# Kernel tuning notes

Measured on AMD Instinct MI355X. Metric: run time of the kernel, lower is better.

The kernel has to match this reference:

```python
import jax, jax.numpy as jnp
import numpy as np

NUM_FINE = 1048576
NUM_FEATURES = 128
TARGET_NUM_SEGMENTS = 262144


def setup_inputs() -> dict:
    key = jax.random.key(0)
    k1, k2 = jax.random.split(key)
    fine_scale_h_d = jax.random.normal(k1, (NUM_FINE, NUM_FEATURES), dtype=jnp.float32)
    prolongation_map_fine_to_coarse = jax.random.randint(
        k2, (NUM_FINE,), 0, TARGET_NUM_SEGMENTS, dtype=jnp.int32)
    return {
        "fine_scale_h_d": fine_scale_h_d,
        "prolongation_map_fine_to_coarse": prolongation_map_fine_to_coarse,
    }


def reference(fine_scale_h_d, prolongation_map_fine_to_coarse):
    # segment_mean = segment_sum / segment_count, with 0 for empty segments
    # (matches tf.math.segment_mean). No sort needed: segment_sum handles
    # unsorted ids via scatter-add, which is the math-equivalent single pass.
    seg_sum = jax.ops.segment_sum(
        fine_scale_h_d, prolongation_map_fine_to_coarse,
        num_segments=TARGET_NUM_SEGMENTS)  # [S, F]
    seg_cnt = jax.ops.segment_sum(
        jnp.ones((fine_scale_h_d.shape[0],), dtype=fine_scale_h_d.dtype),
        prolongation_map_fine_to_coarse,
        num_segments=TARGET_NUM_SEGMENTS)  # [S]
    denom = jnp.maximum(seg_cnt, 1.0)[:, None]
    return seg_sum / denom
```

## Files before the change

kernel.cpp:

```cpp
#include <hip/hip_runtime.h>

#define NUM_FINE 1048576
#define NF 128
#define NUM_SEG 262144

typedef float f32x4 __attribute__((ext_vector_type(4)));

__global__ void count_rank_kernel(const int* __restrict__ ids, int* __restrict__ cnt,
                                  int* __restrict__ rank) {
    int i = (blockIdx.x * blockDim.x + threadIdx.x) * 4;
    int4 a = *reinterpret_cast<const int4*>(ids + i);
    int4 r;
    r.x = atomicAdd(&cnt[a.x], 1);
    r.y = atomicAdd(&cnt[a.y], 1);
    r.z = atomicAdd(&cnt[a.z], 1);
    r.w = atomicAdd(&cnt[a.w], 1);
    *reinterpret_cast<int4*>(rank + i) = r;
}

__global__ void scan1_kernel(const int* __restrict__ cnt, int* __restrict__ base,
                             int* __restrict__ blockSums) {
    __shared__ int lds[256];
    int tid = threadIdx.x;
    int g = blockIdx.x * 1024 + tid * 4;
    int4 a = *reinterpret_cast<const int4*>(cnt + g);
    int s = a.x + a.y + a.z + a.w;
    lds[tid] = s;
    __syncthreads();
    for (int off = 1; off < 256; off <<= 1) {
        int v = (tid >= off) ? lds[tid - off] : 0;
        __syncthreads();
        lds[tid] += v;
        __syncthreads();
    }
    int excl = lds[tid] - s;
    int4 o;
    o.x = excl;
    o.y = o.x + a.x;
    o.z = o.y + a.y;
    o.w = o.z + a.z;
    *reinterpret_cast<int4*>(base + g) = o;
    if (tid == 255) blockSums[blockIdx.x] = lds[255];
}

__global__ void scan3_kernel(int* __restrict__ base, const int* __restrict__ blockSums,
                             const int* __restrict__ cnt, int2* __restrict__ desc) {
    __shared__ int lds[256];
    int tid = threadIdx.x;
    int v = blockSums[tid];
    lds[tid] = v;
    __syncthreads();
    for (int off = 1; off < 256; off <<= 1) {
        int t = (tid >= off) ? lds[tid - off] : 0;
        __syncthreads();
        lds[tid] += t;
        __syncthreads();
    }
    int add = (blockIdx.x > 0) ? lds[blockIdx.x - 1] : 0;
    int g = blockIdx.x * 1024 + tid * 4;
    int4 b = *reinterpret_cast<int4*>(base + g);
    int4 cc = *reinterpret_cast<const int4*>(cnt + g);
    b.x += add; b.y += add; b.z += add; b.w += add;
    *reinterpret_cast<int4*>(base + g) = b;
    *reinterpret_cast<int4*>(desc + g)     = make_int4(b.x, cc.x, b.y, cc.y);
    *reinterpret_cast<int4*>(desc + g + 2) = make_int4(b.z, cc.z, b.w, cc.w);
}

__global__ void place_kernel(const int* __restrict__ ids, const int* __restrict__ base,
                             const int* __restrict__ rank, int* __restrict__ perm) {
    int i = (blockIdx.x * blockDim.x + threadIdx.x) * 4;
    int4 a = *reinterpret_cast<const int4*>(ids + i);
    int4 r = *reinterpret_cast<const int4*>(rank + i);
    perm[base[a.x] + r.x] = i;
    perm[base[a.y] + r.y] = i + 1;
    perm[base[a.z] + r.z] = i + 2;
    perm[base[a.w] + r.w] = i + 3;
}

__device__ __forceinline__ f32x4 rowld(const float* __restrict__ x,
                                       const int* __restrict__ perm,
                                       int j, int end, int last, int f) {
    int jj = (j < end) ? j : last;
    int row = perm[jj];
    f32x4 v = *reinterpret_cast<const f32x4*>(x + (size_t)row * NF + f);
    float m = (j < end) ? 1.f : 0.f;
    return v * m;
}

__global__ void gather_kernel(const float* __restrict__ x,
                              const int* __restrict__ perm,
                              const int2* __restrict__ desc,
                              float* __restrict__ out) {
    int wid = (blockIdx.x << 2) | (threadIdx.x >> 6);
    int lane = threadIdx.x & 63;
    int h = lane >> 5;
    int f = (lane & 31) << 2;
    int2 d = desc[wid];
    int start = d.x, c = d.y;
    int end = start + c, last = end - 1;
    f32x4 acc = {0.f, 0.f, 0.f, 0.f};
    if (c > 0) {
        if (c <= 2) {
            acc = rowld(x, perm, start + h, end, last, f);
        } else if (c <= 4) {
            acc = rowld(x, perm, start + h,     end, last, f)
                + rowld(x, perm, start + 2 + h, end, last, f);
        } else if (c <= 8) {
            acc = rowld(x, perm, start + h,     end, last, f)
                + rowld(x, perm, start + 2 + h, end, last, f)
                + rowld(x, perm, start + 4 + h, end, last, f)
                + rowld(x, perm, start + 6 + h, end, last, f);
        } else {
            for (int r = start; r < end; r += 8) {
                acc += rowld(x, perm, r + h,     end, last, f)
                     + rowld(x, perm, r + 2 + h, end, last, f)
                     + rowld(x, perm, r + 4 + h, end, last, f)
                     + rowld(x, perm, r + 6 + h, end, last, f);
            }
        }
        acc.x += __shfl_xor(acc.x, 32);
        acc.y += __shfl_xor(acc.y, 32);
        acc.z += __shfl_xor(acc.z, 32);
        acc.w += __shfl_xor(acc.w, 32);
    }
    if (h == 0) {
        float inv = 1.0f / (float)(c > 1 ? c : 1);
        f32x4 o = acc * inv;
        *reinterpret_cast<f32x4*>(out + (size_t)wid * NF + f) = o;
    }
}

extern "C" void kernel_launch(void* const* d_in, const int* in_sizes, int n_in,
                              void* d_out, int out_size, void* d_ws, size_t ws_size,
                              hipStream_t stream) {
    const float* x   = (const float*)d_in[0];
    const int*   ids = (const int*)d_in[1];
    float* out = (float*)d_out;

    char* ws = (char*)d_ws;
    int*  cnt       = (int*)(ws);
    int*  base      = (int*)(ws + (1 << 20));
    int*  blockSums = (int*)(ws + (2 << 20));
    int*  perm      = (int*)(ws + (3 << 20));
    int*  rank      = (int*)(ws + (7 << 20));
    int2* desc      = (int2*)(ws + (11 << 20));

    hipMemsetAsync(cnt, 0, (size_t)NUM_SEG * sizeof(int), stream);

    count_rank_kernel<<<NUM_FINE / 1024, 256, 0, stream>>>(ids, cnt, rank);
    scan1_kernel<<<NUM_SEG / 1024, 256, 0, stream>>>(cnt, base, blockSums);
    scan3_kernel<<<NUM_SEG / 1024, 256, 0, stream>>>(base, blockSums, cnt, desc);
    place_kernel<<<NUM_FINE / 1024, 256, 0, stream>>>(ids, base, rank, perm);

    gather_kernel<<<NUM_SEG / 4, 256, 0, stream>>>(x, perm, desc, out);
}
```

Baseline: 209.8 us.

## Fuse counting, scan and placement into one cooperative kernel

Replaces the memset and the four setup kernels (count/rank, two scan passes, place) with a single cooperative kernel of 256 blocks × 512 threads that uses grid-wide syncs between phases. Ranks and ids stay in registers, so the rank array is no longer written to and read back from global memory. Launch overheads go away as well. A 5–6 row case is added to the gather branch to avoid one padded load. The trade-off is grid.sync costs and lower parallelism per phase, since each thread handles 8 ids.

```diff
diff --git a/kernel.cpp b/kernel.cpp
--- a/kernel.cpp
+++ b/kernel.cpp
@@ -1,80 +1,80 @@
 #include <hip/hip_runtime.h>
+#include <hip/hip_cooperative_groups.h>
+
+namespace cg = cooperative_groups;
 
 #define NUM_FINE 1048576
 #define NF 128
 #define NUM_SEG 262144
 
+#define SB 256
+#define ST 512
+
 typedef float f32x4 __attribute__((ext_vector_type(4)));
 
-__global__ void count_rank_kernel(const int* __restrict__ ids, int* __restrict__ cnt,
-                                  int* __restrict__ rank) {
-    int i = (blockIdx.x * blockDim.x + threadIdx.x) * 4;
-    int4 a = *reinterpret_cast<const int4*>(ids + i);
-    int4 r;
-    r.x = atomicAdd(&cnt[a.x], 1);
-    r.y = atomicAdd(&cnt[a.y], 1);
-    r.z = atomicAdd(&cnt[a.z], 1);
-    r.w = atomicAdd(&cnt[a.w], 1);
-    *reinterpret_cast<int4*>(rank + i) = r;
-}
+__global__ void fused_setup(const int* __restrict__ ids, int* __restrict__ cnt,
+                            int* __restrict__ blockSums, int* __restrict__ base,
+                            int* __restrict__ perm, int2* __restrict__ desc) {
+    cg::grid_group grid = cg::this_grid();
+    __shared__ int lds[ST];
+    const int tid = threadIdx.x, bid = blockIdx.x;
+    const int gt = bid * ST + tid;
 
-__global__ void scan1_kernel(const int* __restrict__ cnt, int* __restrict__ base,
-                             int* __restrict__ blockSums) {
-    __shared__ int lds[256];
-    int tid = threadIdx.x;
-    int g = blockIdx.x * 1024 + tid * 4;
-    int4 a = *reinterpret_cast<const int4*>(cnt + g);
-    int s = a.x + a.y + a.z + a.w;
+    *reinterpret_cast<int2*>(cnt + gt * 2) = make_int2(0, 0);
+
+    int myids[8];
+    const int ibase = gt * 8;
+    int4 a0 = *reinterpret_cast<const int4*>(ids + ibase);
+    int4 a1 = *reinterpret_cast<const int4*>(ids + ibase + 4);
+    myids[0] = a0.x; myids[1] = a0.y; myids[2] = a0.z; myids[3] = a0.w;
+    myids[4] = a1.x; myids[5] = a1.y; myids[6] = a1.z; myids[7] = a1.w;
+
+    grid.sync();
+
+    int myrank[8];
+#pragma unroll
+    for (int k = 0; k < 8; ++k) myrank[k] = atomicAdd(&cnt[myids[k]], 1);
+
+    grid.sync();
+
+    const int g = bid * 1024 + tid * 2;
+    int2 c2 = *reinterpret_cast<const int2*>(cnt + g);
+    int s = c2.x + c2.y;
     lds[tid] = s;
     __syncthreads();
-    for (int off = 1; off < 256; off <<= 1) {
+    for (int off = 1; off < ST; off <<= 1) {
         int v = (tid >= off) ? lds[tid - off] : 0;
         __syncthreads();
         lds[tid] += v;
         __syncthreads();
     }
     int excl = lds[tid] - s;
-    int4 o;
-    o.x = excl;
-    o.y = o.x + a.x;
-    o.z = o.y + a.y;
-    o.w = o.z + a.z;
-    *reinterpret_cast<int4*>(base + g) = o;
-    if (tid == 255) blockSums[blockIdx.x] = lds[255];
-}
+    if (tid == 0) blockSums[bid] = lds[ST - 1];
+    grid.sync();
 
-__global__ void scan3_kernel(int* __restrict__ base, const int* __restrict__ blockSums,
-                             const int* __restrict__ cnt, int2* __restrict__ desc) {
-    __shared__ int lds[256];
-    int tid = threadIdx.x;
-    int v = blockSums[tid];
-    lds[tid] = v;
-    __syncthreads();
-    for (int off = 1; off < 256; off <<= 1) {
-        int t = (tid >= off) ? lds[tid - off] : 0;
+    {
+        int v = (tid < SB) ? blockSums[tid] : 0;
         __syncthreads();
-        lds[tid] += t;
+        lds[tid] = v;
         __syncthreads();
+        for (int off = 1; off < SB; off <<= 1) {
+            int t = (tid >= off && tid < SB) ? lds[tid - off] : 0;
+            __syncthreads();
+            if (tid < SB) lds[tid] += t;
+            __syncthreads();
+        }
+        int add = (bid > 0) ? lds[bid - 1] : 0;
+        int b0 = excl + add;
+        int b1 = b0 + c2.x;
+        *reinterpret_cast<int2*>(base + g) = make_int2(b0, b1);
+        *reinterpret_cast<int4*>(desc + g) = make_int4(b0, c2.x, b1, c2.y);
     }
-    int add = (blockIdx.x > 0) ? lds[blockIdx.x - 1] : 0;
-    int g = blockIdx.x * 1024 + tid * 4;
-    int4 b = *reinterpret_cast<int4*>(base + g);
-    int4 cc = *reinterpret_cast<const int4*>(cnt + g);
-    b.x += add; b.y += add; b.z += add; b.w += add;
-    *reinterpret_cast<int4*>(base + g) = b;
-    *reinterpret_cast<int4*>(desc + g)     = make_int4(b.x, cc.x, b.y, cc.y);
-    *reinterpret_cast<int4*>(desc + g + 2) = make_int4(b.z, cc.z, b.w, cc.w);
-}
+    grid.sync();
 
-__global__ void place_kernel(const int* __restrict__ ids, const int* __restrict__ base,
-                             const int* __restrict__ rank, int* __restrict__ perm) {
-    int i = (blockIdx.x * blockDim.x + threadIdx.x) * 4;
-    int4 a = *reinterpret_cast<const int4*>(ids + i);
-    int4 r = *reinterpret_cast<const int4*>(rank + i);
-    perm[base[a.x] + r.x] = i;
-    perm[base[a.y] + r.y] = i + 1;
-    perm[base[a.z] + r.z] = i + 2;
-    perm[base[a.w] + r.w] = i + 3;
+#pragma unroll
+    for (int k = 0; k < 8; ++k) {
+        perm[base[myids[k]] + myrank[k]] = ibase + k;
+    }
 }
 
 __device__ __forceinline__ f32x4 rowld(const float* __restrict__ x,
@@ -105,6 +105,10 @@
         } else if (c <= 4) {
             acc = rowld(x, perm, start + h,     end, last, f)
                 + rowld(x, perm, start + 2 + h, end, last, f);
+        } else if (c <= 6) {
+            acc = rowld(x, perm, start + h,     end, last, f)
+                + rowld(x, perm, start + 2 + h, end, last, f)
+                + rowld(x, perm, start + 4 + h, end, last, f);
         } else if (c <= 8) {
             acc = rowld(x, perm, start + h,     end, last, f)
                 + rowld(x, perm, start + 2 + h, end, last, f)
@@ -141,16 +145,13 @@
     int*  cnt       = (int*)(ws);
     int*  base      = (int*)(ws + (1 << 20));
     int*  blockSums = (int*)(ws + (2 << 20));
-    int*  perm      = (int*)(ws + (3 << 20));
-    int*  rank      = (int*)(ws + (7 << 20));
-    int2* desc      = (int2*)(ws + (11 << 20));
+    int2* desc      = (int2*)(ws + (3 << 20));
+    int*  perm      = (int*)(ws + (5 << 20));
 
-    hipMemsetAsync(cnt, 0, (size_t)NUM_SEG * sizeof(int), stream);
-
-    count_rank_kernel<<<NUM_FINE / 1024, 256, 0, stream>>>(ids, cnt, rank);
-    scan1_kernel<<<NUM_SEG / 1024, 256, 0, stream>>>(cnt, base, blockSums);
-    scan3_kernel<<<NUM_SEG / 1024, 256, 0, stream>>>(base, blockSums, cnt, desc);
-    place_kernel<<<NUM_FINE / 1024, 256, 0, stream>>>(ids, base, rank, perm);
+    void* args[] = {(void*)&ids, (void*)&cnt, (void*)&blockSums,
+                    (void*)&base, (void*)&perm, (void*)&desc};
+    hipLaunchCooperativeKernel((const void*)fused_setup, dim3(SB), dim3(ST),
+                               args, 0, stream);
 
     gather_kernel<<<NUM_SEG / 4, 256, 0, stream>>>(x, perm, desc, out);
 }
```

Result: slower. 321.0 us (+53.0%).
